# Kernel optimization log

Hardware: AMD Instinct MI355X
Metric: run time of the kernel (lower is better)

## Reference

```python
import jax, jax.numpy as jnp
import numpy as np

H = 16
D_MODEL = 1024
D_K = D_MODEL // H


def setup_inputs() -> dict:
    key = jax.random.key(0)
    ks = jax.random.split(key, 11)
    B, S = 4, 2048
    scale = 1.0 / np.sqrt(D_MODEL)
    inp = {
        "query": jax.random.normal(ks[0], (B, S, D_MODEL), dtype=jnp.float32),
        "key": jax.random.normal(ks[1], (B, S, D_MODEL), dtype=jnp.float32),
        "value": jax.random.normal(ks[2], (B, S, D_MODEL), dtype=jnp.float32),
        "Wq": jax.random.normal(ks[3], (D_MODEL, D_MODEL), dtype=jnp.float32) * scale,
        "bq": jnp.zeros((D_MODEL,), dtype=jnp.float32),
        "Wk": jax.random.normal(ks[4], (D_MODEL, D_MODEL), dtype=jnp.float32) * scale,
        "bk": jnp.zeros((D_MODEL,), dtype=jnp.float32),
        "Wv": jax.random.normal(ks[5], (D_MODEL, D_MODEL), dtype=jnp.float32) * scale,
        "bv": jnp.zeros((D_MODEL,), dtype=jnp.float32),
        "Wo": jax.random.normal(ks[6], (D_MODEL, D_MODEL), dtype=jnp.float32) * scale,
        "bo": jnp.zeros((D_MODEL,), dtype=jnp.float32),
    }
    return inp


def reference(query, key, value, Wq, bq, Wk, bk, Wv, bv, Wo, bo):
    B, S, _ = query.shape

    def proj(x, W, b):
        # nn.Linear: x @ W.T + b, then split heads -> [B, H, S, D_K]
        y = jnp.einsum("bsd,ed->bse", x, W) + b
        return y.reshape(B, S, H, D_K).transpose(0, 2, 1, 3)

    q = proj(query, Wq, bq)
    k = proj(key, Wk, bk)
    v = proj(value, Wv, bv)

    scores = jnp.einsum("bhqd,bhkd->bhqk", q, k) / jnp.sqrt(jnp.float32(D_K))
    attn = jax.nn.softmax(scores, axis=-1)
    out = jnp.einsum("bhqk,bhkd->bhqd", attn, v)  # [B,H,S,D_K]
    out = out.transpose(0, 2, 1, 3).reshape(B, S, H * D_K)
    # final linear (dropout disabled in eval / deterministic reference)
    return jnp.einsum("bsd,ed->bse", out, Wo) + bo
```

## Files before the change

### kernel.cpp

```cpp
#include <hip/hip_runtime.h>
#include <stdint.h>

typedef __attribute__((ext_vector_type(8))) short short8;
typedef __attribute__((ext_vector_type(4))) float floatx4;
typedef __attribute__((ext_vector_type(16))) float floatx16;

#define DEV __device__ __forceinline__

DEV unsigned short f2bf(float x) {
  unsigned u = __float_as_uint(x);
  u += 0x7fffu + ((u >> 16) & 1u);
  return (unsigned short)(u >> 16);
}

DEV unsigned pkbf(float hi, float lo) {
  return __builtin_amdgcn_perm(__float_as_uint(hi) + 0x8000u,
                               __float_as_uint(lo) + 0x8000u, 0x07060302u);
}

DEV unsigned cvtpk(float a, float b) {
  unsigned r;
  asm("v_cvt_pk_bf16_f32 %0, %1, %2" : "=v"(r) : "v"(a), "v"(b));
  return r;
}

DEV short8 pack4(unsigned a0, unsigned a1, unsigned b0, unsigned b1) {
  union { unsigned u[4]; short8 s; } t;
  t.u[0] = a0; t.u[1] = a1; t.u[2] = b0; t.u[3] = b1;
  return t.s;
}

DEV void load_lds16(const unsigned short* g, unsigned short* l) {
  __builtin_amdgcn_global_load_lds(
      (const __attribute__((address_space(1))) void*)g,
      (__attribute__((address_space(3))) void*)l, 16, 0, 0);
}

DEV void lds_fence() { asm volatile("" ::: "memory"); }

#define ASM_VMCNT(n) asm volatile("s_waitcnt vmcnt(" #n ")" ::: "memory")
DEV void sched_fence() { __builtin_amdgcn_sched_barrier(0); }

__global__ void cvt_all(const float* __restrict__ Wq, const float* __restrict__ Wk,
                        const float* __restrict__ Wv, const float* __restrict__ Wo,
                        const float* __restrict__ Xq, const float* __restrict__ Xk,
                        const float* __restrict__ Xv,
                        unsigned short* __restrict__ Wb, unsigned short* __restrict__ XqB,
                        unsigned short* __restrict__ XkB, unsigned short* __restrict__ XvB) {
  int bid = blockIdx.x;
  const float* src;
  unsigned short* dst;
  int off;
  if (bid < 4096) {
    int sel = bid >> 10;
    src = sel == 0 ? Wq : sel == 1 ? Wk : sel == 2 ? Wv : Wo;
    dst = Wb + (size_t)sel * 1048576;
    off = bid & 1023;
  } else {
    bid -= 4096;
    int sel = bid >> 13;
    src = sel == 0 ? Xq : sel == 1 ? Xk : Xv;
    dst = sel == 0 ? XqB : sel == 1 ? XkB : XvB;
    off = bid & 8191;
  }
  int i = (off * 256 + threadIdx.x) * 4;
  float4 v = *(const float4*)(src + i);
  uint2 o;
  o.x = pkbf(v.y, v.x);
  o.y = pkbf(v.w, v.z);
  *(uint2*)(dst + i) = o;
}

#define SCQ (0.125f * 1.44269504089f)
__global__ __launch_bounds__(256, 3) void qkv_gemm(
    const unsigned short* __restrict__ XqB, const unsigned short* __restrict__ XkB,
    const unsigned short* __restrict__ XvB,
    const unsigned short* __restrict__ Wb,
    const float* __restrict__ bq, const float* __restrict__ bk, const float* __restrict__ bv,
    unsigned short* __restrict__ Qp, unsigned short* __restrict__ Kp,
    unsigned short* __restrict__ VTp) {
  __shared__ alignas(16) unsigned short Xs[3][128 * 32];
  __shared__ alignas(16) unsigned short Ws[3][128 * 32];
  const int z = blockIdx.z;
  const unsigned short* X = z == 0 ? XqB : z == 1 ? XkB : XvB;
  const unsigned short* W = Wb + (size_t)z * 1048576;
  const float* bias = z == 0 ? bq : z == 1 ? bk : bv;

  const int tid = threadIdx.x;
  const int lane = tid & 63, wave = tid >> 6;
  const int lcol = lane & 15, quad = lane >> 4;
  const int n2 = blockIdx.x + 8 * blockIdx.y;
  const int xcd = n2 & 7, ii = n2 >> 3;
  const int wo = (ii >> 3) * 128;
  const int xo = (xcd * 8 + (ii & 7)) * 128;
  const int wm = (wave & 1) * 64;
  const int wn = (wave >> 1) * 64;

  floatx4 acc[4][4];
  for (int mi = 0; mi < 4; ++mi)
    for (int ni = 0; ni < 4; ++ni)
      for (int r = 0; r < 4; ++r) acc[mi][ni][r] = 0.f;

  auto stage = [&](int kt, int buf) {
    const int k0 = kt * 32;
    int c = tid;
    load_lds16(W + (size_t)(wo + (c >> 2)) * 1024 + k0 + (c & 3) * 8, Ws[buf] + c * 8);
    load_lds16(X + (size_t)(xo + (c >> 2)) * 1024 + k0 + (c & 3) * 8, Xs[buf] + c * 8);
    c = tid + 256;
    load_lds16(W + (size_t)(wo + (c >> 2)) * 1024 + k0 + (c & 3) * 8, Ws[buf] + c * 8);
    load_lds16(X + (size_t)(xo + (c >> 2)) * 1024 + k0 + (c & 3) * 8, Xs[buf] + c * 8);
  };

  stage(0, 0);
  stage(1, 1);
  int cur = 0;
  for (int kt = 0; kt < 32; ++kt) {
    sched_fence();
    ASM_VMCNT(4);
    __builtin_amdgcn_s_barrier();
    sched_fence();
    int nb = cur + 2; if (nb >= 3) nb -= 3;
    stage((kt + 2) & 31, nb);
    const unsigned short* Ab = (z < 2) ? Ws[cur] : Xs[cur];
    const unsigned short* Bb = (z < 2) ? Xs[cur] : Ws[cur];
    short8 af[4], bfr[4];
#pragma unroll
    for (int mi = 0; mi < 4; ++mi)
      af[mi] = *(const short8*)(Ab + (wm + mi * 16 + lcol) * 32 + quad * 8);
#pragma unroll
    for (int ni = 0; ni < 4; ++ni)
      bfr[ni] = *(const short8*)(Bb + (wn + ni * 16 + lcol) * 32 + quad * 8);
#pragma unroll
    for (int mi = 0; mi < 4; ++mi)
#pragma unroll
      for (int ni = 0; ni < 4; ++ni)
        acc[mi][ni] = __builtin_amdgcn_mfma_f32_16x16x32_bf16(af[mi], bfr[ni], acc[mi][ni], 0, 0, 0);
    cur = (cur == 2) ? 0 : cur + 1;
  }

  if (z < 2) {
    unsigned short* Out = z == 0 ? Qp : Kp;
    const float scl = z == 0 ? SCQ : 1.f;
#pragma unroll
    for (int mi = 0; mi < 4; ++mi) {
      int dbase = wo + wm + mi * 16 + quad * 4;
      float4 bv4 = *(const float4*)(bias + dbase);
      int h = dbase >> 6, dk = dbase & 63;
#pragma unroll
      for (int ni = 0; ni < 4; ++ni) {
        int sg = xo + wn + ni * 16 + lcol;
        int bb = sg >> 11, ss = sg & 2047;
        uint2 o;
        o.x = pkbf((acc[mi][ni][1] + bv4.y) * scl, (acc[mi][ni][0] + bv4.x) * scl);
        o.y = pkbf((acc[mi][ni][3] + bv4.w) * scl, (acc[mi][ni][2] + bv4.z) * scl);
        *(uint2*)(Out + ((size_t)(bb * 16 + h) * 2048 + ss) * 64 + dk) = o;
      }
    }
  } else {
#pragma unroll
    for (int ni = 0; ni < 4; ++ni) {
      int dg = wo + wn + ni * 16 + lcol;
      float bvx = bias[dg];
      int h = dg >> 6, dk = dg & 63;
#pragma unroll
      for (int mi = 0; mi < 4; ++mi) {
        int sbase = xo + wm + mi * 16 + quad * 4;
        int bb = sbase >> 11, ss = sbase & 2047;
        uint2 o;
        o.x = pkbf(acc[mi][ni][1] + bvx, acc[mi][ni][0] + bvx);
        o.y = pkbf(acc[mi][ni][3] + bvx, acc[mi][ni][2] + bvx);
        *(uint2*)(VTp + ((size_t)(bb * 16 + h) * 64 + dk) * 2048 + ss) = o;
      }
    }
  }
}

__global__ __launch_bounds__(256, 3) void gemm_o(
    const unsigned short* __restrict__ A, const unsigned short* __restrict__ Bw,
    const float* __restrict__ bias, float* __restrict__ Out) {
  __shared__ alignas(16) unsigned short Cs[3][128 * 32];
  __shared__ alignas(16) unsigned short Wos[3][128 * 32];
  const int tid = threadIdx.x;
  const int lane = tid & 63, wave = tid >> 6;
  const int lcol = lane & 15, quad = lane >> 4;
  const int n2 = blockIdx.x + 8 * blockIdx.y;
  const int xcd = n2 & 7, ii = n2 >> 3;
  const int co = (ii >> 3) * 128;
  const int so = (xcd * 8 + (ii & 7)) * 128;
  const int wm = (wave & 1) * 64;
  const int wn = (wave >> 1) * 64;

  floatx4 acc[4][4];
  for (int mi = 0; mi < 4; ++mi)
    for (int ni = 0; ni < 4; ++ni)
      for (int r = 0; r < 4; ++r) acc[mi][ni][r] = 0.f;

  auto stage = [&](int kt, int buf) {
    const int k0 = kt * 32;
    int c = tid;
    load_lds16(Bw + (size_t)(co + (c >> 2)) * 1024 + k0 + (c & 3) * 8, Wos[buf] + c * 8);
    load_lds16(A  + (size_t)(so + (c >> 2)) * 1024 + k0 + (c & 3) * 8, Cs[buf] + c * 8);
    c = tid + 256;
    load_lds16(Bw + (size_t)(co + (c >> 2)) * 1024 + k0 + (c & 3) * 8, Wos[buf] + c * 8);
    load_lds16(A  + (size_t)(so + (c >> 2)) * 1024 + k0 + (c & 3) * 8, Cs[buf] + c * 8);
  };

  stage(0, 0);
  stage(1, 1);
  int cur = 0;
  for (int kt = 0; kt < 32; ++kt) {
    sched_fence();
    ASM_VMCNT(4);
    __builtin_amdgcn_s_barrier();
    sched_fence();
    int nb = cur + 2; if (nb >= 3) nb -= 3;
    stage((kt + 2) & 31, nb);
    short8 af[4], bfr[4];
#pragma unroll
    for (int mi = 0; mi < 4; ++mi)
      af[mi] = *(const short8*)(Wos[cur] + (wm + mi * 16 + lcol) * 32 + quad * 8);
#pragma unroll
    for (int ni = 0; ni < 4; ++ni)
      bfr[ni] = *(const short8*)(Cs[cur] + (wn + ni * 16 + lcol) * 32 + quad * 8);
#pragma unroll
    for (int mi = 0; mi < 4; ++mi)
#pragma unroll
      for (int ni = 0; ni < 4; ++ni)
        acc[mi][ni] = __builtin_amdgcn_mfma_f32_16x16x32_bf16(af[mi], bfr[ni], acc[mi][ni], 0, 0, 0);
    cur = (cur == 2) ? 0 : cur + 1;
  }
#pragma unroll
  for (int mi = 0; mi < 4; ++mi) {
    int cb = co + wm + mi * 16 + quad * 4;
    float4 bv4 = *(const float4*)(bias + cb);
#pragma unroll
    for (int ni = 0; ni < 4; ++ni) {
      int sg = so + wn + ni * 16 + lcol;
      float4 o;
      o.x = acc[mi][ni][0] + bv4.x;
      o.y = acc[mi][ni][1] + bv4.y;
      o.z = acc[mi][ni][2] + bv4.z;
      o.w = acc[mi][ni][3] + bv4.w;
      *(float4*)(Out + (size_t)sg * 1024 + cb) = o;
    }
  }
}

__global__ __launch_bounds__(256, 3) void attn_kernel(
    const unsigned short* __restrict__ Qp, const unsigned short* __restrict__ Kp,
    const unsigned short* __restrict__ VTp, unsigned short* __restrict__ Ctx) {
  __shared__ alignas(16) unsigned short Ks[3][64 * 64];
  __shared__ alignas(16) unsigned short Vt[3][64 * 64];

  const int tid = threadIdx.x;
  const int lane = tid & 63, wave = tid >> 6;
  const int l31 = lane & 31, hh = lane >> 5;
  const int wq = wave * 32;
  const int n = blockIdx.x + 16 * (blockIdx.y + 16 * blockIdx.z);
  const int xcd = n & 7, ii = n >> 3;
  const int hb = xcd * 8 + (ii & 7);
  const int qt = ii >> 3;
  const size_t bh = (size_t)hb * 2048 * 64;
  const int b = hb >> 4;
  const unsigned short* Qb = Qp + bh + (size_t)qt * 128 * 64;
  const unsigned short* Kb = Kp + bh;
  const unsigned short* VTb = VTp + bh;

  short8 qf[4];
#pragma unroll
  for (int st = 0; st < 4; ++st)
    qf[st] = *(const short8*)(Qb + (wq + l31) * 64 + st * 16 + hh * 8);

  auto stageK = [&](int jt, int buf) {
#pragma unroll
    for (int i = 0; i < 2; ++i) {
      int p = tid + i * 256;
      int kr = p >> 3, kj = p & 7;
      load_lds16(Kb + (size_t)jt * 4096 + kr * 64 + ((kj ^ (kr & 7)) * 8), Ks[buf] + p * 8);
    }
  };
  auto stageV = [&](int jt, int buf) {
#pragma unroll
    for (int i = 0; i < 2; ++i) {
      int p = tid + i * 256;
      int vr = p >> 3, vj = p & 7;
      load_lds16(VTb + (size_t)vr * 2048 + jt * 64 + ((vj ^ (vr & 7)) * 8), Vt[buf] + p * 8);
    }
  };

  stageK(0, 0); stageV(0, 0);
  stageK(1, 1); stageV(1, 1);
  __syncthreads();

  short8 ones;
#pragma unroll
  for (int j = 0; j < 8; ++j) ones[j] = (short)0x3f80;

  float M = -1e30f;
  floatx16 Oacc[2], OaccL;
#pragma unroll
  for (int r = 0; r < 16; ++r) { Oacc[0][r] = 0.f; Oacc[1][r] = 0.f; OaccL[r] = 0.f; }

  int cur = 0;
  for (int jt = 0; jt < 32; ++jt) {
    int nb = cur + 2; if (nb >= 3) nb -= 3;
    const int jn = (jt + 2) & 31;
    stageK(jn, nb);
    stageV(jn, nb);

    const unsigned short* Kc = Ks[cur];
    floatx16 sacc[2];
#pragma unroll
    for (int r = 0; r < 16; ++r) { sacc[0][r] = 0.f; sacc[1][r] = 0.f; }
#pragma unroll
    for (int st = 0; st < 4; ++st)
#pragma unroll
      for (int mk = 0; mk < 2; ++mk) {
        int row = mk * 32 + l31;
        short8 kf = *(const short8*)(Kc + row * 64 + (((2 * st + hh) ^ (row & 7)) * 8));
        sacc[mk] = __builtin_amdgcn_mfma_f32_32x32x16_bf16(kf, qf[st], sacc[mk], 0, 0, 0);
      }

    float t8[8];
#pragma unroll
    for (int r = 0; r < 8; ++r)
      t8[r] = fmaxf(fmaxf(sacc[0][r], sacc[0][r + 8]), fmaxf(sacc[1][r], sacc[1][r + 8]));
    float t4a = fmaxf(t8[0], t8[4]), t4b = fmaxf(t8[1], t8[5]);
    float t4c = fmaxf(t8[2], t8[6]), t4d = fmaxf(t8[3], t8[7]);
    float mloc = fmaxf(fmaxf(t4a, t4b), fmaxf(t4c, t4d));
    float m2 = fmaxf(mloc, __shfl_xor(mloc, 32));

    const int skip = __all(m2 <= M + 8.f);
    if (!skip) {
      float mnew = fmaxf(M, m2);
      float alpha = exp2f(M - mnew);
      M = mnew;
#pragma unroll
      for (int r = 0; r < 16; ++r) {
        int srcl = (r & 3) + 8 * (r >> 2) + hh * 4;
        float ar = __shfl(alpha, srcl);
        Oacc[0][r] *= ar;
        Oacc[1][r] *= ar;
        OaccL[r] *= ar;
      }
    }
#pragma unroll
    for (int mk = 0; mk < 2; ++mk)
#pragma unroll
      for (int r = 0; r < 16; ++r) sacc[mk][r] = exp2f(sacc[mk][r] - M);

    unsigned wpk[2][4][2];
#pragma unroll
    for (int mk = 0; mk < 2; ++mk)
#pragma unroll
      for (int c = 0; c < 4; ++c) {
        wpk[mk][c][0] = cvtpk(sacc[mk][4 * c + 0], sacc[mk][4 * c + 1]);
        wpk[mk][c][1] = cvtpk(sacc[mk][4 * c + 2], sacc[mk][4 * c + 3]);
      }

    const unsigned short* Vc = Vt[cur];
#pragma unroll
    for (int kk = 0; kk < 4; ++kk) {
      const int e = kk & 1, mk = kk >> 1;
      unsigned a0 = wpk[mk][2 * e][0], b0 = wpk[mk][2 * e + 1][0];
      unsigned a1 = wpk[mk][2 * e][1], b1 = wpk[mk][2 * e + 1][1];
      asm("v_permlane32_swap_b32 %0, %1" : "+v"(a0), "+v"(b0));
      asm("v_permlane32_swap_b32 %0, %1" : "+v"(a1), "+v"(b1));
      short8 pa = pack4(a0, a1, b0, b1);
#pragma unroll
      for (int nd = 0; nd < 2; ++nd) {
        int row = nd * 32 + l31;
        short8 vf = *(const short8*)(Vc + row * 64 + (((2 * kk + hh) ^ (row & 7)) * 8));
        Oacc[nd] = __builtin_amdgcn_mfma_f32_32x32x16_bf16(pa, vf, Oacc[nd], 0, 0, 0);
      }
      OaccL = __builtin_amdgcn_mfma_f32_32x32x16_bf16(pa, ones, OaccL, 0, 0, 0);
    }

    sched_fence();
    ASM_VMCNT(4);
    __builtin_amdgcn_s_barrier();
    sched_fence();
    cur = (cur == 2) ? 0 : cur + 1;
  }

  ASM_VMCNT(0);
  __syncthreads();
  unsigned short* Obuf = &Ks[0][0];
  float linv[16];
#pragma unroll
  for (int r = 0; r < 16; ++r) linv[r] = 1.f / OaccL[r];
#pragma unroll
  for (int nd = 0; nd < 2; ++nd)
#pragma unroll
    for (int r = 0; r < 16; ++r) {
      int q = wq + (r & 3) + 8 * (r >> 2) + hh * 4;
      int d = nd * 32 + l31;
      Obuf[q * 64 + (((d >> 3) ^ (q & 7)) * 8) + (d & 7)] = f2bf(Oacc[nd][r] * linv[r]);
    }
  __syncthreads();
#pragma unroll
  for (int i = 0; i < 4; ++i) {
    int c = tid + i * 256;
    int row = c >> 3, pj = c & 7;
    uint4 v = *(const uint4*)(Obuf + row * 64 + ((pj ^ (row & 7)) * 8));
    *(uint4*)(Ctx + ((size_t)(b * 2048 + qt * 128 + row)) * 1024 + (hb & 15) * 64 + pj * 8) = v;
  }
}

extern "C" void kernel_launch(void* const* d_in, const int* in_sizes, int n_in,
                              void* d_out, int out_size, void* d_ws, size_t ws_size,
                              hipStream_t stream) {
  const float* query = (const float*)d_in[0];
  const float* key_  = (const float*)d_in[1];
  const float* value = (const float*)d_in[2];
  const float* Wq = (const float*)d_in[3];
  const float* bq = (const float*)d_in[4];
  const float* Wk = (const float*)d_in[5];
  const float* bk = (const float*)d_in[6];
  const float* Wv = (const float*)d_in[7];
  const float* bv = (const float*)d_in[8];
  const float* Wo = (const float*)d_in[9];
  const float* bo = (const float*)d_in[10];

  char* w = (char*)d_ws;
  unsigned short* Wb  = (unsigned short*)w; w += (size_t)4 * 1024 * 1024 * 2;
  unsigned short* Qp  = (unsigned short*)w; w += (size_t)8192 * 1024 * 2;
  unsigned short* Kp  = (unsigned short*)w; w += (size_t)8192 * 1024 * 2;
  unsigned short* VTp = (unsigned short*)w; w += (size_t)8192 * 1024 * 2;
  unsigned short* Ctx = (unsigned short*)w; w += (size_t)8192 * 1024 * 2;

  unsigned short* XqB = (unsigned short*)d_out;
  unsigned short* XkB = (unsigned short*)d_out + (size_t)8192 * 1024;
  unsigned short* XvB = Ctx;

  cvt_all<<<28672, 256, 0, stream>>>(Wq, Wk, Wv, Wo, query, key_, value,
                                     Wb, XqB, XkB, XvB);

  qkv_gemm<<<dim3(8, 64, 3), 256, 0, stream>>>(XqB, XkB, XvB, Wb,
                                               bq, bk, bv, Qp, Kp, VTp);

  attn_kernel<<<dim3(16, 16, 4), 256, 0, stream>>>(Qp, Kp, VTp, Ctx);

  gemm_o<<<dim3(8, 64), 256, 0, stream>>>(Ctx, Wb + (size_t)3 * 1048576, bo, (float*)d_out);
}
```

Measured before the change: 375.6 us.

## Fuse fp32-to-bf16 conversion into GEMM staging and drop separate convert kernel

```diff
diff --git a/kernel.cpp b/kernel.cpp
--- a/kernel.cpp
+++ b/kernel.cpp
@@ -36,54 +36,26 @@
       (__attribute__((address_space(3))) void*)l, 16, 0, 0);
 }
 
-DEV void lds_fence() { asm volatile("" ::: "memory"); }
-
 #define ASM_VMCNT(n) asm volatile("s_waitcnt vmcnt(" #n ")" ::: "memory")
+#define ASM_LGKM0() asm volatile("s_waitcnt lgkmcnt(0)" ::: "memory")
 DEV void sched_fence() { __builtin_amdgcn_sched_barrier(0); }
 
-__global__ void cvt_all(const float* __restrict__ Wq, const float* __restrict__ Wk,
-                        const float* __restrict__ Wv, const float* __restrict__ Wo,
-                        const float* __restrict__ Xq, const float* __restrict__ Xk,
-                        const float* __restrict__ Xv,
-                        unsigned short* __restrict__ Wb, unsigned short* __restrict__ XqB,
-                        unsigned short* __restrict__ XkB, unsigned short* __restrict__ XvB) {
-  int bid = blockIdx.x;
-  const float* src;
-  unsigned short* dst;
-  int off;
-  if (bid < 4096) {
-    int sel = bid >> 10;
-    src = sel == 0 ? Wq : sel == 1 ? Wk : sel == 2 ? Wv : Wo;
-    dst = Wb + (size_t)sel * 1048576;
-    off = bid & 1023;
-  } else {
-    bid -= 4096;
-    int sel = bid >> 13;
-    src = sel == 0 ? Xq : sel == 1 ? Xk : Xv;
-    dst = sel == 0 ? XqB : sel == 1 ? XkB : XvB;
-    off = bid & 8191;
-  }
-  int i = (off * 256 + threadIdx.x) * 4;
-  float4 v = *(const float4*)(src + i);
-  uint2 o;
-  o.x = pkbf(v.y, v.x);
-  o.y = pkbf(v.w, v.z);
-  *(uint2*)(dst + i) = o;
+DEV short8 fragld(const unsigned short* buf, int row, int quad) {
+  return *(const short8*)(buf + row * 32 + ((quad ^ ((row >> 1) & 3)) * 8));
 }
 
 #define SCQ (0.125f * 1.44269504089f)
 __global__ __launch_bounds__(256, 3) void qkv_gemm(
-    const unsigned short* __restrict__ XqB, const unsigned short* __restrict__ XkB,
-    const unsigned short* __restrict__ XvB,
-    const unsigned short* __restrict__ Wb,
+    const float* __restrict__ Xq, const float* __restrict__ Xk, const float* __restrict__ Xv,
+    const float* __restrict__ Wqw, const float* __restrict__ Wkw, const float* __restrict__ Wvw,
     const float* __restrict__ bq, const float* __restrict__ bk, const float* __restrict__ bv,
     unsigned short* __restrict__ Qp, unsigned short* __restrict__ Kp,
     unsigned short* __restrict__ VTp) {
-  __shared__ alignas(16) unsigned short Xs[3][128 * 32];
-  __shared__ alignas(16) unsigned short Ws[3][128 * 32];
+  __shared__ alignas(16) unsigned short Xs[2][128 * 32];
+  __shared__ alignas(16) unsigned short Ws[2][128 * 32];
   const int z = blockIdx.z;
-  const unsigned short* X = z == 0 ? XqB : z == 1 ? XkB : XvB;
-  const unsigned short* W = Wb + (size_t)z * 1048576;
+  const float* X = z == 0 ? Xq : z == 1 ? Xk : Xv;
+  const float* W = z == 0 ? Wqw : z == 1 ? Wkw : Wvw;
   const float* bias = z == 0 ? bq : z == 1 ? bk : bv;
 
   const int tid = threadIdx.x;
@@ -96,46 +68,70 @@
   const int wm = (wave & 1) * 64;
   const int wn = (wave >> 1) * 64;
 
+  const int srow = tid >> 1, half = tid & 1;
+  const float* Xrow = X + (size_t)(xo + srow) * 1024 + half * 16;
+  const float* Wrow = W + (size_t)(wo + srow) * 1024 + half * 16;
+  const int ssw = (srow >> 1) & 3;
+
+  float4 rx[4], rw[4];
+  auto issue = [&](int kt) {
+    const int k0 = kt * 32;
+#pragma unroll
+    for (int j = 0; j < 4; ++j) {
+      rx[j] = *(const float4*)(Xrow + k0 + j * 4);
+      rw[j] = *(const float4*)(Wrow + k0 + j * 4);
+    }
+  };
+  auto writeT = [&](int buf) {
+#pragma unroll
+    for (int e = 0; e < 2; ++e) {
+      int ch = half * 2 + e;
+      unsigned x0 = cvtpk(rx[2 * e].x, rx[2 * e].y);
+      unsigned x1 = cvtpk(rx[2 * e].z, rx[2 * e].w);
+      unsigned x2 = cvtpk(rx[2 * e + 1].x, rx[2 * e + 1].y);
+      unsigned x3 = cvtpk(rx[2 * e + 1].z, rx[2 * e + 1].w);
+      *(short8*)(Xs[buf] + srow * 32 + ((ch ^ ssw) * 8)) = pack4(x0, x1, x2, x3);
+      unsigned w0 = cvtpk(rw[2 * e].x, rw[2 * e].y);
+      unsigned w1 = cvtpk(rw[2 * e].z, rw[2 * e].w);
+      unsigned w2 = cvtpk(rw[2 * e + 1].x, rw[2 * e + 1].y);
+      unsigned w3 = cvtpk(rw[2 * e + 1].z, rw[2 * e + 1].w);
+      *(short8*)(Ws[buf] + srow * 32 + ((ch ^ ssw) * 8)) = pack4(w0, w1, w2, w3);
+    }
+  };
+
   floatx4 acc[4][4];
   for (int mi = 0; mi < 4; ++mi)
     for (int ni = 0; ni < 4; ++ni)
       for (int r = 0; r < 4; ++r) acc[mi][ni][r] = 0.f;
 
-  auto stage = [&](int kt, int buf) {
-    const int k0 = kt * 32;
-    int c = tid;
-    load_lds16(W + (size_t)(wo + (c >> 2)) * 1024 + k0 + (c & 3) * 8, Ws[buf] + c * 8);
-    load_lds16(X + (size_t)(xo + (c >> 2)) * 1024 + k0 + (c & 3) * 8, Xs[buf] + c * 8);
-    c = tid + 256;
-    load_lds16(W + (size_t)(wo + (c >> 2)) * 1024 + k0 + (c & 3) * 8, Ws[buf] + c * 8);
-    load_lds16(X + (size_t)(xo + (c >> 2)) * 1024 + k0 + (c & 3) * 8, Xs[buf] + c * 8);
-  };
-
-  stage(0, 0);
-  stage(1, 1);
-  int cur = 0;
+  issue(0);
+  writeT(0);
+  issue(1);
+  ASM_LGKM0();
+  sched_fence();
+  __builtin_amdgcn_s_barrier();
+  sched_fence();
+
   for (int kt = 0; kt < 32; ++kt) {
-    sched_fence();
-    ASM_VMCNT(4);
-    __builtin_amdgcn_s_barrier();
-    sched_fence();
-    int nb = cur + 2; if (nb >= 3) nb -= 3;
-    stage((kt + 2) & 31, nb);
+    const int cur = kt & 1;
     const unsigned short* Ab = (z < 2) ? Ws[cur] : Xs[cur];
     const unsigned short* Bb = (z < 2) ? Xs[cur] : Ws[cur];
     short8 af[4], bfr[4];
 #pragma unroll
-    for (int mi = 0; mi < 4; ++mi)
-      af[mi] = *(const short8*)(Ab + (wm + mi * 16 + lcol) * 32 + quad * 8);
-#pragma unroll
-    for (int ni = 0; ni < 4; ++ni)
-      bfr[ni] = *(const short8*)(Bb + (wn + ni * 16 + lcol) * 32 + quad * 8);
+    for (int mi = 0; mi < 4; ++mi) af[mi] = fragld(Ab, wm + mi * 16 + lcol, quad);
+#pragma unroll
+    for (int ni = 0; ni < 4; ++ni) bfr[ni] = fragld(Bb, wn + ni * 16 + lcol, quad);
 #pragma unroll
     for (int mi = 0; mi < 4; ++mi)
 #pragma unroll
       for (int ni = 0; ni < 4; ++ni)
         acc[mi][ni] = __builtin_amdgcn_mfma_f32_16x16x32_bf16(af[mi], bfr[ni], acc[mi][ni], 0, 0, 0);
-    cur = (cur == 2) ? 0 : cur + 1;
+    writeT(cur ^ 1);
+    issue((kt + 2) & 31);
+    ASM_LGKM0();
+    sched_fence();
+    __builtin_amdgcn_s_barrier();
+    sched_fence();
   }
 
   if (z < 2) {
@@ -176,10 +172,10 @@
 }
 
 __global__ __launch_bounds__(256, 3) void gemm_o(
-    const unsigned short* __restrict__ A, const unsigned short* __restrict__ Bw,
+    const unsigned short* __restrict__ A, const float* __restrict__ Wo,
     const float* __restrict__ bias, float* __restrict__ Out) {
-  __shared__ alignas(16) unsigned short Cs[3][128 * 32];
-  __shared__ alignas(16) unsigned short Wos[3][128 * 32];
+  __shared__ alignas(16) unsigned short Cs[2][128 * 32];
+  __shared__ alignas(16) unsigned short Wos[2][128 * 32];
   const int tid = threadIdx.x;
   const int lane = tid & 63, wave = tid >> 6;
   const int lcol = lane & 15, quad = lane >> 4;
@@ -190,44 +186,64 @@
   const int wm = (wave & 1) * 64;
   const int wn = (wave >> 1) * 64;
 
+  const int srow = tid >> 1, half = tid & 1;
+  const unsigned short* Crow = A + (size_t)(so + srow) * 1024 + half * 16;
+  const float* Wrow = Wo + (size_t)(co + srow) * 1024 + half * 16;
+  const int ssw = (srow >> 1) & 3;
+
+  uint4 rc[2];
+  float4 rw[4];
+  auto issue = [&](int kt) {
+    const int k0 = kt * 32;
+#pragma unroll
+    for (int j = 0; j < 2; ++j) rc[j] = *(const uint4*)(Crow + k0 + j * 8);
+#pragma unroll
+    for (int j = 0; j < 4; ++j) rw[j] = *(const float4*)(Wrow + k0 + j * 4);
+  };
+  auto writeT = [&](int buf) {
+#pragma unroll
+    for (int e = 0; e < 2; ++e) {
+      int ch = half * 2 + e;
+      *(uint4*)(Cs[buf] + srow * 32 + ((ch ^ ssw) * 8)) = rc[e];
+      unsigned w0 = cvtpk(rw[2 * e].x, rw[2 * e].y);
+      unsigned w1 = cvtpk(rw[2 * e].z, rw[2 * e].w);
+      unsigned w2 = cvtpk(rw[2 * e + 1].x, rw[2 * e + 1].y);
+      unsigned w3 = cvtpk(rw[2 * e + 1].z, rw[2 * e + 1].w);
+      *(short8*)(Wos[buf] + srow * 32 + ((ch ^ ssw) * 8)) = pack4(w0, w1, w2, w3);
+    }
+  };
+
   floatx4 acc[4][4];
   for (int mi = 0; mi < 4; ++mi)
     for (int ni = 0; ni < 4; ++ni)
       for (int r = 0; r < 4; ++r) acc[mi][ni][r] = 0.f;
 
-  auto stage = [&](int kt, int buf) {
-    const int k0 = kt * 32;
-    int c = tid;
-    load_lds16(Bw + (size_t)(co + (c >> 2)) * 1024 + k0 + (c & 3) * 8, Wos[buf] + c * 8);
-    load_lds16(A  + (size_t)(so + (c >> 2)) * 1024 + k0 + (c & 3) * 8, Cs[buf] + c * 8);
-    c = tid + 256;
-    load_lds16(Bw + (size_t)(co + (c >> 2)) * 1024 + k0 + (c & 3) * 8, Wos[buf] + c * 8);
-    load_lds16(A  + (size_t)(so + (c >> 2)) * 1024 + k0 + (c & 3) * 8, Cs[buf] + c * 8);
-  };
-
-  stage(0, 0);
-  stage(1, 1);
-  int cur = 0;
+  issue(0);
+  writeT(0);
+  issue(1);
+  ASM_LGKM0();
+  sched_fence();
+  __builtin_amdgcn_s_barrier();
+  sched_fence();
+
   for (int kt = 0; kt < 32; ++kt) {
-    sched_fence();
-    ASM_VMCNT(4);
-    __builtin_amdgcn_s_barrier();
-    sched_fence();
-    int nb = cur + 2; if (nb >= 3) nb -= 3;
-    stage((kt + 2) & 31, nb);
+    const int cur = kt & 1;
     short8 af[4], bfr[4];
 #pragma unroll
-    for (int mi = 0; mi < 4; ++mi)
-      af[mi] = *(const short8*)(Wos[cur] + (wm + mi * 16 + lcol) * 32 + quad * 8);
-#pragma unroll
-    for (int ni = 0; ni < 4; ++ni)
-      bfr[ni] = *(const short8*)(Cs[cur] + (wn + ni * 16 + lcol) * 32 + quad * 8);
+    for (int mi = 0; mi < 4; ++mi) af[mi] = fragld(Wos[cur], wm + mi * 16 + lcol, quad);
+#pragma unroll
+    for (int ni = 0; ni < 4; ++ni) bfr[ni] = fragld(Cs[cur], wn + ni * 16 + lcol, quad);
 #pragma unroll
     for (int mi = 0; mi < 4; ++mi)
 #pragma unroll
       for (int ni = 0; ni < 4; ++ni)
         acc[mi][ni] = __builtin_amdgcn_mfma_f32_16x16x32_bf16(af[mi], bfr[ni], acc[mi][ni], 0, 0, 0);
-    cur = (cur == 2) ? 0 : cur + 1;
+    writeT(cur ^ 1);
+    issue((kt + 2) & 31);
+    ASM_LGKM0();
+    sched_fence();
+    __builtin_amdgcn_s_barrier();
+    sched_fence();
   }
 #pragma unroll
   for (int mi = 0; mi < 4; ++mi) {
@@ -271,21 +287,18 @@
   for (int st = 0; st < 4; ++st)
     qf[st] = *(const short8*)(Qb + (wq + l31) * 64 + st * 16 + hh * 8);
 
+  const int p0 = tid, p1 = tid + 256;
+  const int ko0 = (p0 >> 3) * 64 + (((p0 & 7) ^ ((p0 >> 3) & 7)) * 8);
+  const int ko1 = (p1 >> 3) * 64 + (((p1 & 7) ^ ((p1 >> 3) & 7)) * 8);
+  const int vo0 = (p0 >> 3) * 2048 + (((p0 & 7) ^ ((p0 >> 3) & 7)) * 8);
+  const int vo1 = (p1 >> 3) * 2048 + (((p1 & 7) ^ ((p1 >> 3) & 7)) * 8);
   auto stageK = [&](int jt, int buf) {
-#pragma unroll
-    for (int i = 0; i < 2; ++i) {
-      int p = tid + i * 256;
-      int kr = p >> 3, kj = p & 7;
-      load_lds16(Kb + (size_t)jt * 4096 + kr * 64 + ((kj ^ (kr & 7)) * 8), Ks[buf] + p * 8);
-    }
+    load_lds16(Kb + (size_t)jt * 4096 + ko0, Ks[buf] + p0 * 8);
+    load_lds16(Kb + (size_t)jt * 4096 + ko1, Ks[buf] + p1 * 8);
   };
   auto stageV = [&](int jt, int buf) {
-#pragma unroll
-    for (int i = 0; i < 2; ++i) {
-      int p = tid + i * 256;
-      int vr = p >> 3, vj = p & 7;
-      load_lds16(VTb + (size_t)vr * 2048 + jt * 64 + ((vj ^ (vr & 7)) * 8), Vt[buf] + p * 8);
-    }
+    load_lds16(VTb + vo0 + jt * 64, Vt[buf] + p0 * 8);
+    load_lds16(VTb + vo1 + jt * 64, Vt[buf] + p1 * 8);
   };
 
   stageK(0, 0); stageV(0, 0);
@@ -295,6 +308,9 @@
   short8 ones;
 #pragma unroll
   for (int j = 0; j < 8; ++j) ones[j] = (short)0x3f80;
+  floatx16 z16;
+#pragma unroll
+  for (int r = 0; r < 16; ++r) z16[r] = 0.f;
 
   float M = -1e30f;
   floatx16 Oacc[2], OaccL;
@@ -311,9 +327,13 @@
     const unsigned short* Kc = Ks[cur];
     floatx16 sacc[2];
 #pragma unroll
-    for (int r = 0; r < 16; ++r) { sacc[0][r] = 0.f; sacc[1][r] = 0.f; }
-#pragma unroll
-    for (int st = 0; st < 4; ++st)
+    for (int mk = 0; mk < 2; ++mk) {
+      int row = mk * 32 + l31;
+      short8 kf = *(const short8*)(Kc + row * 64 + ((hh ^ (row & 7)) * 8));
+      sacc[mk] = __builtin_amdgcn_mfma_f32_32x32x16_bf16(kf, qf[0], z16, 0, 0, 0);
+    }
+#pragma unroll
+    for (int st = 1; st < 4; ++st)
 #pragma unroll
       for (int mk = 0; mk < 2; ++mk) {
         int row = mk * 32 + l31;
@@ -423,23 +443,15 @@
   const float* bo = (const float*)d_in[10];
 
   char* w = (char*)d_ws;
-  unsigned short* Wb  = (unsigned short*)w; w += (size_t)4 * 1024 * 1024 * 2;
   unsigned short* Qp  = (unsigned short*)w; w += (size_t)8192 * 1024 * 2;
   unsigned short* Kp  = (unsigned short*)w; w += (size_t)8192 * 1024 * 2;
   unsigned short* VTp = (unsigned short*)w; w += (size_t)8192 * 1024 * 2;
   unsigned short* Ctx = (unsigned short*)w; w += (size_t)8192 * 1024 * 2;
 
-  unsigned short* XqB = (unsigned short*)d_out;
-  unsigned short* XkB = (unsigned short*)d_out + (size_t)8192 * 1024;
-  unsigned short* XvB = Ctx;
-
-  cvt_all<<<28672, 256, 0, stream>>>(Wq, Wk, Wv, Wo, query, key_, value,
-                                     Wb, XqB, XkB, XvB);
-
-  qkv_gemm<<<dim3(8, 64, 3), 256, 0, stream>>>(XqB, XkB, XvB, Wb,
+  qkv_gemm<<<dim3(8, 64, 3), 256, 0, stream>>>(query, key_, value, Wq, Wk, Wv,
                                                bq, bk, bv, Qp, Kp, VTp);
 
   attn_kernel<<<dim3(16, 16, 4), 256, 0, stream>>>(Qp, Kp, VTp, Ctx);
 
-  gemm_o<<<dim3(8, 64), 256, 0, stream>>>(Ctx, Wb + (size_t)3 * 1048576, bo, (float*)d_out);
-}
+  gemm_o<<<dim3(8, 64), 256, 0, stream>>>(Ctx, Wo, bo, (float*)d_out);
+}
```

Result: slower. 444.5 us (+18.3%).
